# Performance work log

Hardware: AMD Instinct MI355X
Metric: run time of the kernel (lower is better)

## Reference

```python
import jax, jax.numpy as jnp
import numpy as np

B, C, T, F = 16, 64, 500, 32
G = 8
GF = F // G            # 4 freqs per group
OC = GF * 64           # per-group hidden size = 256
IN = GF * C            # per-group input size = 256


def setup_inputs() -> dict:
    key = jax.random.key(0)
    k1, k2, k3, k4, k5 = jax.random.split(key, 5)
    scale = 1.0 / np.sqrt(OC)
    return {
        "x": jax.random.normal(k1, (B, C, T, F), dtype=jnp.float32),
        "weight_ih": jax.random.normal(k2, (G, 3 * OC, IN), dtype=jnp.float32) * scale,
        "weight_hh": jax.random.normal(k3, (G, 3 * OC, OC), dtype=jnp.float32) * scale,
        "bias_ih": jax.random.normal(k4, (G, 3 * OC), dtype=jnp.float32) * scale,
        "bias_hh": jax.random.normal(k5, (G, 3 * OC), dtype=jnp.float32) * scale,
    }


def reference(x, weight_ih, weight_hh, bias_ih, bias_hh):
    b, c, t, f = x.shape
    g = weight_ih.shape[0]
    oc = weight_ih.shape[1] // 3
    gf = f // g
    # [B,C,T,F] -> [B,T,F,C] -> [B,T,G,gf*C]
    xi = jnp.transpose(x, (0, 2, 3, 1)).reshape(b, t, g, gf * c)
    # input projection for all timesteps at once: [B,T,G,3*OC]
    ih = jnp.einsum('btgi,goi->btgo', xi, weight_ih) + bias_ih

    h0 = jnp.zeros((b, g, oc), dtype=x.dtype)

    def step(h, ih_t):
        hh = jnp.einsum('bgo,gpo->bgp', h, weight_hh) + bias_hh
        ri, zi, ni = jnp.split(ih_t, 3, axis=-1)
        rh, zh, nh = jnp.split(hh, 3, axis=-1)
        r = jax.nn.sigmoid(ri + rh)
        z = jax.nn.sigmoid(zi + zh)
        n = jnp.tanh(ni + r * nh)
        h_new = (1 - z) * n + z * h
        return h_new, h_new

    h_last, hs = jax.lax.scan(step, h0, jnp.swapaxes(ih, 0, 1))  # hs: [T,B,G,OC]
    out = jnp.transpose(hs, (1, 0, 2, 3))                # [B,T,G,OC]
    out = out.reshape(b, t, g, gf, oc // gf)             # unflatten OC -> (gf, out_ch)
    out = out.reshape(b, t, f, oc // gf)                 # merge (G,gf) -> F
    out = jnp.transpose(out, (0, 3, 1, 2))               # [B,out_ch,T,F]
    return out, h_last
```

## Files before the change

kernel.cpp:

```cpp
#include <hip/hip_runtime.h>

typedef _Float16 f16;
typedef _Float16 f16x4 __attribute__((ext_vector_type(4)));
typedef _Float16 f16x8 __attribute__((ext_vector_type(8)));
typedef float    f32x4 __attribute__((ext_vector_type(4)));

#if defined(__has_builtin)
#if __has_builtin(__builtin_amdgcn_fdot2)
#define HAVE_FDOT2 1
#endif
#endif

__device__ __forceinline__ float dot8(f16x8 a, f16x8 b, float acc) {
#ifdef HAVE_FDOT2
  acc = __builtin_amdgcn_fdot2(__builtin_shufflevector(a, a, 0, 1),
                               __builtin_shufflevector(b, b, 0, 1), acc, false);
  acc = __builtin_amdgcn_fdot2(__builtin_shufflevector(a, a, 2, 3),
                               __builtin_shufflevector(b, b, 2, 3), acc, false);
  acc = __builtin_amdgcn_fdot2(__builtin_shufflevector(a, a, 4, 5),
                               __builtin_shufflevector(b, b, 4, 5), acc, false);
  acc = __builtin_amdgcn_fdot2(__builtin_shufflevector(a, a, 6, 7),
                               __builtin_shufflevector(b, b, 6, 7), acc, false);
#else
  #pragma unroll
  for (int i = 0; i < 8; i++) acc += (float)a[i] * (float)b[i];
#endif
  return acc;
}

__global__ void k_pack_x(const float* __restrict__ x, f16* __restrict__ xi) {
  const int tc = blockIdx.x;
  const int b  = blockIdx.y;
  const int t0 = tc * 4;
  const int tid = threadIdx.x;
  __shared__ __align__(16) float lds[64 * 133];
  #pragma unroll
  for (int it = 0; it < 32; it++) {
    int flat = it * 256 + tid;
    int c = flat >> 7;
    int t = (flat >> 5) & 3;
    int f = flat & 31;
    lds[c * 133 + t * 33 + f] =
        x[(((size_t)b * 64 + c) * 500 + t0 + t) * 32 + f];
  }
  __syncthreads();
  const int w = tid >> 6, l = tid & 63;
  #pragma unroll
  for (int rr = 0; rr < 8; rr++) {
    int row = w * 8 + rr;
    int g = row >> 2, t = row & 3;
    f16x4 v;
    #pragma unroll
    for (int e = 0; e < 4; e++) {
      int i = l * 4 + e;
      int gf = i >> 6, c = i & 63;
      v[e] = (f16)lds[c * 133 + t * 33 + g * 4 + gf];
    }
    *(f16x4*)&xi[((size_t)g * 8000 + (size_t)b * 500 + t0 + t) * 256 + l * 4] = v;
  }
}

__global__ void k_pack_wih(const float* __restrict__ w, f16* __restrict__ wh) {
  size_t i0 = ((size_t)blockIdx.x * 256 + threadIdx.x) * 8;
  f32x4 a = *(const f32x4*)(w + i0);
  f32x4 b = *(const f32x4*)(w + i0 + 4);
  f16x8 v;
  v[0]=(f16)a[0]; v[1]=(f16)a[1]; v[2]=(f16)a[2]; v[3]=(f16)a[3];
  v[4]=(f16)b[0]; v[5]=(f16)b[1]; v[6]=(f16)b[2]; v[7]=(f16)b[3];
  *(f16x8*)(wh + i0) = v;
}

__global__ void k_pack_whh(const float* __restrict__ w, f16* __restrict__ wp) {
  const int j = blockIdx.x;
  const int g = blockIdx.y;
  const int tid = threadIdx.x;
  const int q = j >> 4, kb = j & 15;
  const int row = q * 256 + (tid >> 1);
  const int k0  = (tid & 1) * 128 + kb * 8;
  const float* src = w + ((size_t)g * 768 + row) * 256 + k0;
  f16x8 v;
  #pragma unroll
  for (int e = 0; e < 8; e++) v[e] = (f16)src[e];
  *(f16x8*)&wp[(((size_t)g * 48 + j) * 512 + tid) * 8] = v;
}

__global__ __launch_bounds__(256) void k_gemm(const f16* __restrict__ xi,
                                              const f16* __restrict__ wih,
                                              const float* __restrict__ bias,
                                              f16* __restrict__ ih) {
  const int mt = blockIdx.x;
  const int nt = blockIdx.y;
  const int g  = blockIdx.z;
  const int tid = threadIdx.x;
  const int w = tid >> 6, l = tid & 63;
  __shared__ __align__(16) f16 Als[64 * 64];
  __shared__ __align__(16) f16 Bls[128 * 64];
  f32x4 zero = {0.f, 0.f, 0.f, 0.f};
  f32x4 acc[4][2];
  #pragma unroll
  for (int mi = 0; mi < 4; mi++)
    #pragma unroll
    for (int ni = 0; ni < 2; ni++) acc[mi][ni] = zero;

  const int arow = tid >> 2, aq = tid & 3;
  const int brow = tid >> 1, bq = tid & 1;
  for (int kk = 0; kk < 4; kk++) {
    const f16* asrc = xi + ((size_t)g * 8000 + mt * 64 + arow) * 256 + kk * 64 + aq * 16;
    f16x8 a0 = *(const f16x8*)asrc;
    f16x8 a1 = *(const f16x8*)(asrc + 8);
    *(f16x8*)&Als[arow * 64 + ((aq * 2 + 0) ^ (arow & 7)) * 8] = a0;
    *(f16x8*)&Als[arow * 64 + ((aq * 2 + 1) ^ (arow & 7)) * 8] = a1;
    const f16* bsrc = wih + ((size_t)g * 768 + nt * 128 + brow) * 256 + kk * 64 + bq * 32;
    #pragma unroll
    for (int jj = 0; jj < 4; jj++) {
      f16x8 v = *(const f16x8*)(bsrc + jj * 8);
      *(f16x8*)&Bls[brow * 64 + ((bq * 4 + jj) ^ (brow & 7)) * 8] = v;
    }
    __syncthreads();
    #pragma unroll
    for (int ks = 0; ks < 2; ks++) {
      f16x8 af[4], bf[2];
      #pragma unroll
      for (int mi = 0; mi < 4; mi++) {
        int r = mi * 16 + (l & 15);
        af[mi] = *(const f16x8*)&Als[r * 64 + ((ks * 4 + (l >> 4)) ^ (r & 7)) * 8];
      }
      #pragma unroll
      for (int ni = 0; ni < 2; ni++) {
        int r = w * 32 + ni * 16 + (l & 15);
        bf[ni] = *(const f16x8*)&Bls[r * 64 + ((ks * 4 + (l >> 4)) ^ (r & 7)) * 8];
      }
      #pragma unroll
      for (int mi = 0; mi < 4; mi++)
        #pragma unroll
        for (int ni = 0; ni < 2; ni++)
          acc[mi][ni] = __builtin_amdgcn_mfma_f32_16x16x32_f16(af[mi], bf[ni], acc[mi][ni], 0, 0, 0);
    }
    __syncthreads();
  }
  #pragma unroll
  for (int ni = 0; ni < 2; ni++) {
    int col = nt * 128 + w * 32 + ni * 16 + (l & 15);
    float bs = bias[g * 768 + col];
    #pragma unroll
    for (int mi = 0; mi < 4; mi++) {
      int m0 = mt * 64 + mi * 16 + (l >> 4) * 4;
      #pragma unroll
      for (int e = 0; e < 4; e++) {
        ih[((size_t)g * 8000 + m0 + e) * 768 + col] = (f16)(acc[mi][ni][e] + bs);
      }
    }
  }
}

__global__ __launch_bounds__(512, 2)
__attribute__((amdgpu_waves_per_eu(2, 2)))
void k_recur(const f16* __restrict__ ih,
             const f16* __restrict__ wp,
             const float* __restrict__ bias_hh,
             f16* __restrict__ hs,
             float* __restrict__ hlast) {
  const int g = blockIdx.x;
  const int b = blockIdx.y;
  const int tid = threadIdx.x;
  const int r2 = tid >> 1;
  const int kc = tid & 1;
  __shared__ __align__(16) f16 hsm[2][264];

  const f16x8* wsrc = (const f16x8*)wp + (size_t)g * 48 * 512 + tid;
#define WL(J) f16x8 w##J = wsrc[(size_t)(J) * 512]; \
              asm volatile("" : "+v"(w##J));
  WL(0)  WL(1)  WL(2)  WL(3)  WL(4)  WL(5)  WL(6)  WL(7)
  WL(8)  WL(9)  WL(10) WL(11) WL(12) WL(13) WL(14) WL(15)
  WL(16) WL(17) WL(18) WL(19) WL(20) WL(21) WL(22) WL(23)
  WL(24) WL(25) WL(26) WL(27) WL(28) WL(29) WL(30) WL(31)
  WL(32) WL(33) WL(34) WL(35) WL(36) WL(37) WL(38) WL(39)
  WL(40) WL(41) WL(42) WL(43) WL(44) WL(45) WL(46) WL(47)
#undef WL

  const float bh0 = bias_hh[g * 768 + r2];
  const float bh1 = bias_hh[g * 768 + 256 + r2];
  const float bh2 = bias_hh[g * 768 + 512 + r2];
  const f16* ihb = ih + ((size_t)g * 8000 + (size_t)b * 500) * 768;
  f16* hsp = hs + (size_t)(b * 8 + g) * 500 * 256;
  const int wslot = r2 + ((r2 >> 7) << 3);
  float hreg = 0.f;
  f16 c0 = ihb[r2], c1 = ihb[256 + r2], c2 = ihb[512 + r2];
  if (tid < 256) hsm[0][tid + ((tid >> 7) << 3)] = (f16)0.f;
  __syncthreads();

#define DOT4(KB, WA0, WA1, WA2, WA3, WB0, WB1, WB2, WB3, WC0, WC1, WC2, WC3) \
  {                                                                          \
    f16x8 h0 = hv[(KB) + 0], h1 = hv[(KB) + 1];                              \
    f16x8 h2 = hv[(KB) + 2], h3 = hv[(KB) + 3];                              \
    a0 = dot8(WA0, h0, a0); a1 = dot8(WB0, h0, a1); a2 = dot8(WC0, h0, a2);  \
    a0 = dot8(WA1, h1, a0); a1 = dot8(WB1, h1, a1); a2 = dot8(WC1, h1, a2);  \
    a0 = dot8(WA2, h2, a0); a1 = dot8(WB2, h2, a1); a2 = dot8(WC2, h2, a2);  \
    a0 = dot8(WA3, h3, a0); a1 = dot8(WB3, h3, a1); a2 = dot8(WC3, h3, a2);  \
    __builtin_amdgcn_sched_barrier(0);                                       \
  }

  int cur = 0;
  for (int t = 0; t < 500; t++) {
    f16 n0 = c0, n1 = c1, n2 = c2;
    if (t + 1 < 500) {
      const f16* p = ihb + (size_t)(t + 1) * 768;
      n0 = p[r2]; n1 = p[256 + r2]; n2 = p[512 + r2];
    }
    float a0 = 0.f, a1 = 0.f, a2 = 0.f;
    const f16x8* hv = (const f16x8*)&hsm[cur][kc * 136];
    DOT4(0,  w0,  w1,  w2,  w3,  w16, w17, w18, w19, w32, w33, w34, w35)
    DOT4(4,  w4,  w5,  w6,  w7,  w20, w21, w22, w23, w36, w37, w38, w39)
    DOT4(8,  w8,  w9,  w10, w11, w24, w25, w26, w27, w40, w41, w42, w43)
    DOT4(12, w12, w13, w14, w15, w28, w29, w30, w31, w44, w45, w46, w47)
    a0 += __shfl_xor(a0, 1, 64);
    a1 += __shfl_xor(a1, 1, 64);
    a2 += __shfl_xor(a2, 1, 64);
    float r = 1.f / (1.f + __expf(-((float)c0 + a0 + bh0)));
    float z = 1.f / (1.f + __expf(-((float)c1 + a1 + bh1)));
    float nx = (float)c2 + r * (a2 + bh2);
    float n = 2.f / (1.f + __expf(-2.f * nx)) - 1.f;
    float hn = (1.f - z) * n + z * hreg;
    hreg = hn;
    if (kc == 0) {
      hsm[cur ^ 1][wslot] = (f16)hn;
      hsp[(size_t)t * 256 + r2] = (f16)hn;
    }
    __syncthreads();
    cur ^= 1;
    c0 = n0; c1 = n1; c2 = n2;
  }
  if (kc == 0) hlast[(size_t)(b * 8 + g) * 256 + r2] = hreg;
#undef DOT4
}

__global__ void k_untr(const f16* __restrict__ hs, float* __restrict__ out) {
  const int tc = blockIdx.x;
  const int b  = blockIdx.y;
  const int t0 = tc * 8;
  const int tid = threadIdx.x;
  __shared__ __align__(16) f16 lds[8 * 8 * 260];
  {
    const int row = tid >> 2, q = tid & 3;
    const int g = row >> 3, tt = row & 7;
    if (t0 + tt < 500) {
      const f16* src = hs + (((size_t)b * 8 + g) * 500 + t0 + tt) * 256 + q * 64;
      #pragma unroll
      for (int jj = 0; jj < 16; jj++) {
        *(f16x4*)&lds[(tt * 8 + g) * 260 + q * 64 + jj * 4] = *(const f16x4*)(src + jj * 4);
      }
    }
  }
  __syncthreads();
  const int w = tid >> 6, l = tid & 63;
  const int tt2 = w * 2 + (l >> 5);
  const int f = l & 31;
  const int gg = f >> 2, gf = f & 3;
  if (t0 + tt2 < 500) {
    float* dst = out + (((size_t)b * 64) * 500 + t0 + tt2) * 32 + f;
    const f16* srcl = &lds[(tt2 * 8 + gg) * 260 + gf * 64];
    #pragma unroll 4
    for (int och = 0; och < 64; och++) {
      dst[(size_t)och * 500 * 32] = (float)srcl[och];
    }
  }
}

extern "C" void kernel_launch(void* const* d_in, const int* in_sizes, int n_in,
                              void* d_out, int out_size, void* d_ws, size_t ws_size,
                              hipStream_t stream) {
  const float* x   = (const float*)d_in[0];
  const float* wih = (const float*)d_in[1];
  const float* whh = (const float*)d_in[2];
  const float* bih = (const float*)d_in[3];
  const float* bhh = (const float*)d_in[4];
  float* out   = (float*)d_out;
  float* hlast = out + 16384000;

  char* ws = (char*)d_ws;
  f16* ih_h  = (f16*)(ws);
  f16* xi_h  = (f16*)(ws + 98304000);
  f16* wih_h = (f16*)(ws + 131072000);
  f16* whh_p = (f16*)(ws + 134217728);
  f16* hs_h  = (f16*)(ws + 137363456);

  k_pack_x  <<<dim3(125, 16), 256, 0, stream>>>(x, xi_h);
  k_pack_wih<<<768, 256, 0, stream>>>(wih, wih_h);
  k_pack_whh<<<dim3(48, 8), 512, 0, stream>>>(whh, whh_p);
  k_gemm    <<<dim3(125, 6, 8), 256, 0, stream>>>(xi_h, wih_h, bih, ih_h);
  k_recur   <<<dim3(8, 16), 512, 0, stream>>>(ih_h, whh_p, bhh, hs_h, hlast);
  k_untr    <<<dim3(63, 16), 256, 0, stream>>>(hs_h, out);
}
```

Baseline: 729.6 us.

## Split recurrent hidden-state dot products across four lanes per row

The GRU recurrence kernel now uses 1024 threads per block, with four lanes sharing each hidden unit instead of two. Each lane holds 24 instead of 48 register-resident weight vectors and performs half as many dot products per timestep. The partial sums are combined with two xor shuffles. The weight packing layout and the shared-memory layout of h are changed to match. The aim is to shorten the serial per-step critical path by adding parallelism, at the cost of an extra shuffle stage and a barrier across 16 waves instead of 8.

After: 861.3 us. 18.0% more time.

```diff
diff --git a/kernel.cpp b/kernel.cpp
--- a/kernel.cpp
+++ b/kernel.cpp
@@ -74,14 +74,14 @@
   const int j = blockIdx.x;
   const int g = blockIdx.y;
   const int tid = threadIdx.x;
-  const int q = j >> 4, kb = j & 15;
-  const int row = q * 256 + (tid >> 1);
-  const int k0  = (tid & 1) * 128 + kb * 8;
+  const int gi = j >> 3, kb = j & 7;
+  const int row = gi * 256 + (tid >> 2);
+  const int k0  = (tid & 3) * 64 + kb * 8;
   const float* src = w + ((size_t)g * 768 + row) * 256 + k0;
   f16x8 v;
   #pragma unroll
   for (int e = 0; e < 8; e++) v[e] = (f16)src[e];
-  *(f16x8*)&wp[(((size_t)g * 48 + j) * 512 + tid) * 8] = v;
+  *(f16x8*)&wp[(((size_t)g * 24 + j) * 1024 + tid) * 8] = v;
 }
 
 __global__ __launch_bounds__(256) void k_gemm(const f16* __restrict__ xi,
@@ -153,8 +153,7 @@
   }
 }
 
-__global__ __launch_bounds__(512, 2)
-__attribute__((amdgpu_waves_per_eu(2, 2)))
+__global__ __launch_bounds__(1024, 4)
 void k_recur(const f16* __restrict__ ih,
              const f16* __restrict__ wp,
              const float* __restrict__ bias_hh,
@@ -163,41 +162,35 @@
   const int g = blockIdx.x;
   const int b = blockIdx.y;
   const int tid = threadIdx.x;
-  const int r2 = tid >> 1;
-  const int kc = tid & 1;
-  __shared__ __align__(16) f16 hsm[2][264];
-
-  const f16x8* wsrc = (const f16x8*)wp + (size_t)g * 48 * 512 + tid;
-#define WL(J) f16x8 w##J = wsrc[(size_t)(J) * 512]; \
+  const int r4 = tid >> 2;
+  const int kc = tid & 3;
+  __shared__ __align__(16) f16 hsm[2][544];
+
+  const f16x8* wsrc = (const f16x8*)wp + (size_t)g * 24 * 1024 + tid;
+#define WL(J) f16x8 w##J = wsrc[(size_t)(J) * 1024]; \
               asm volatile("" : "+v"(w##J));
   WL(0)  WL(1)  WL(2)  WL(3)  WL(4)  WL(5)  WL(6)  WL(7)
   WL(8)  WL(9)  WL(10) WL(11) WL(12) WL(13) WL(14) WL(15)
   WL(16) WL(17) WL(18) WL(19) WL(20) WL(21) WL(22) WL(23)
-  WL(24) WL(25) WL(26) WL(27) WL(28) WL(29) WL(30) WL(31)
-  WL(32) WL(33) WL(34) WL(35) WL(36) WL(37) WL(38) WL(39)
-  WL(40) WL(41) WL(42) WL(43) WL(44) WL(45) WL(46) WL(47)
 #undef WL
 
-  const float bh0 = bias_hh[g * 768 + r2];
-  const float bh1 = bias_hh[g * 768 + 256 + r2];
-  const float bh2 = bias_hh[g * 768 + 512 + r2];
+  const float bh0 = bias_hh[g * 768 + r4];
+  const float bh1 = bias_hh[g * 768 + 256 + r4];
+  const float bh2 = bias_hh[g * 768 + 512 + r4];
   const f16* ihb = ih + ((size_t)g * 8000 + (size_t)b * 500) * 768;
   f16* hsp = hs + (size_t)(b * 8 + g) * 500 * 256;
-  const int wslot = r2 + ((r2 >> 7) << 3);
+  const int wslot = (r4 >> 6) * 136 + (r4 & 63);
   float hreg = 0.f;
-  f16 c0 = ihb[r2], c1 = ihb[256 + r2], c2 = ihb[512 + r2];
-  if (tid < 256) hsm[0][tid + ((tid >> 7) << 3)] = (f16)0.f;
+  f16 c0 = ihb[r4], c1 = ihb[256 + r4], c2 = ihb[512 + r4];
+  if (tid < 256) hsm[0][(tid >> 6) * 136 + (tid & 63)] = (f16)0.f;
   __syncthreads();
 
-#define DOT4(KB, WA0, WA1, WA2, WA3, WB0, WB1, WB2, WB3, WC0, WC1, WC2, WC3) \
-  {                                                                          \
-    f16x8 h0 = hv[(KB) + 0], h1 = hv[(KB) + 1];                              \
-    f16x8 h2 = hv[(KB) + 2], h3 = hv[(KB) + 3];                              \
-    a0 = dot8(WA0, h0, a0); a1 = dot8(WB0, h0, a1); a2 = dot8(WC0, h0, a2);  \
-    a0 = dot8(WA1, h1, a0); a1 = dot8(WB1, h1, a1); a2 = dot8(WC1, h1, a2);  \
-    a0 = dot8(WA2, h2, a0); a1 = dot8(WB2, h2, a1); a2 = dot8(WC2, h2, a2);  \
-    a0 = dot8(WA3, h3, a0); a1 = dot8(WB3, h3, a1); a2 = dot8(WC3, h3, a2);  \
-    __builtin_amdgcn_sched_barrier(0);                                       \
+#define DOTC(KB, WA0, WA1, WB0, WB1, WC0, WC1)                              \
+  {                                                                         \
+    f16x8 h0 = hv[(KB) + 0], h1 = hv[(KB) + 1];                             \
+    a0 = dot8(WA0, h0, a0); a1 = dot8(WB0, h0, a1); a2 = dot8(WC0, h0, a2); \
+    a0 = dot8(WA1, h1, a0); a1 = dot8(WB1, h1, a1); a2 = dot8(WC1, h1, a2); \
+    __builtin_amdgcn_sched_barrier(0);                                      \
   }
 
   int cur = 0;
@@ -205,17 +198,17 @@
     f16 n0 = c0, n1 = c1, n2 = c2;
     if (t + 1 < 500) {
       const f16* p = ihb + (size_t)(t + 1) * 768;
-      n0 = p[r2]; n1 = p[256 + r2]; n2 = p[512 + r2];
+      n0 = p[r4]; n1 = p[256 + r4]; n2 = p[512 + r4];
     }
     float a0 = 0.f, a1 = 0.f, a2 = 0.f;
     const f16x8* hv = (const f16x8*)&hsm[cur][kc * 136];
-    DOT4(0,  w0,  w1,  w2,  w3,  w16, w17, w18, w19, w32, w33, w34, w35)
-    DOT4(4,  w4,  w5,  w6,  w7,  w20, w21, w22, w23, w36, w37, w38, w39)
-    DOT4(8,  w8,  w9,  w10, w11, w24, w25, w26, w27, w40, w41, w42, w43)
-    DOT4(12, w12, w13, w14, w15, w28, w29, w30, w31, w44, w45, w46, w47)
-    a0 += __shfl_xor(a0, 1, 64);
-    a1 += __shfl_xor(a1, 1, 64);
-    a2 += __shfl_xor(a2, 1, 64);
+    DOTC(0, w0, w1, w8,  w9,  w16, w17)
+    DOTC(2, w2, w3, w10, w11, w18, w19)
+    DOTC(4, w4, w5, w12, w13, w20, w21)
+    DOTC(6, w6, w7, w14, w15, w22, w23)
+    a0 += __shfl_xor(a0, 1, 64); a0 += __shfl_xor(a0, 2, 64);
+    a1 += __shfl_xor(a1, 1, 64); a1 += __shfl_xor(a1, 2, 64);
+    a2 += __shfl_xor(a2, 1, 64); a2 += __shfl_xor(a2, 2, 64);
     float r = 1.f / (1.f + __expf(-((float)c0 + a0 + bh0)));
     float z = 1.f / (1.f + __expf(-((float)c1 + a1 + bh1)));
     float nx = (float)c2 + r * (a2 + bh2);
@@ -224,14 +217,14 @@
     hreg = hn;
     if (kc == 0) {
       hsm[cur ^ 1][wslot] = (f16)hn;
-      hsp[(size_t)t * 256 + r2] = (f16)hn;
+      hsp[(size_t)t * 256 + r4] = (f16)hn;
     }
     __syncthreads();
     cur ^= 1;
     c0 = n0; c1 = n1; c2 = n2;
   }
-  if (kc == 0) hlast[(size_t)(b * 8 + g) * 256 + r2] = hreg;
-#undef DOT4
+  if (kc == 0) hlast[(size_t)(b * 8 + g) * 256 + r4] = hreg;
+#undef DOTC
 }
 
 __global__ void k_untr(const f16* __restrict__ hs, float* __restrict__ out) {
@@ -286,8 +279,8 @@
 
   k_pack_x  <<<dim3(125, 16), 256, 0, stream>>>(x, xi_h);
   k_pack_wih<<<768, 256, 0, stream>>>(wih, wih_h);
-  k_pack_whh<<<dim3(48, 8), 512, 0, stream>>>(whh, whh_p);
+  k_pack_whh<<<dim3(24, 8), 1024, 0, stream>>>(whh, whh_p);
   k_gemm    <<<dim3(125, 6, 8), 256, 0, stream>>>(xi_h, wih_h, bih, ih_h);
-  k_recur   <<<dim3(8, 16), 512, 0, stream>>>(ih_h, whh_p, bhh, hs_h, hlast);
+  k_recur   <<<dim3(8, 16), 1024, 0, stream>>>(ih_h, whh_p, bhh, hs_h, hlast);
   k_untr    <<<dim3(63, 16), 256, 0, stream>>>(hs_h, out);
 }
```
